# Optimization experiments

Measured on AMD Instinct MI355X. Metric: run time of the kernel, lower is better.

Reference implementation:

```python
import jax, jax.numpy as jnp
import numpy as np

DS = 8  # avg-pool / upsample factor

def _avg_pool(x, ds):
    B, C, H, W = x.shape
    return x.reshape(B, C, H // ds, ds, W // ds, ds).mean(axis=(3, 5))

def _conv1x1(x, W, b):
    # 1x1 conv == per-pixel channel matmul
    return jnp.einsum('bchw,oc->bohw', x, W) + b[None, :, None, None]

def setup_inputs() -> dict:
    key = jax.random.key(0)
    ks = jax.random.split(key, 8)
    B, C, H, W = 8, 64, 256, 256
    scale = 1.0 / np.sqrt(C)
    return {
        'x':    jax.random.normal(ks[0], (B, C, H, W), dtype=jnp.float32),
        'diff': jax.random.normal(ks[1], (B, C, H, W), dtype=jnp.float32),
        'Wq': jax.random.normal(ks[2], (C, C), dtype=jnp.float32) * scale,
        'bq': jax.random.normal(ks[3], (C,), dtype=jnp.float32) * 0.01,
        'Wk': jax.random.normal(ks[4], (C, C), dtype=jnp.float32) * scale,
        'bk': jax.random.normal(ks[5], (C,), dtype=jnp.float32) * 0.01,
        'Wv': jax.random.normal(ks[6], (C, C), dtype=jnp.float32) * scale,
        'bv': jax.random.normal(ks[7], (C,), dtype=jnp.float32) * 0.01,
    }

def reference(x, diff, Wq, bq, Wk, bk, Wv, bv):
    C = x.shape[1]
    d = _avg_pool(diff, DS)                 # [B,C,h,w]
    B, _, h, w = d.shape
    N = h * w
    q = _conv1x1(d, Wq, bq).reshape(B, C, N)
    k = _conv1x1(d, Wk, bk).reshape(B, C, N)
    # energy[b,n,m] = sum_c q[b,c,n] * k[b,c,m], scaled by C^-0.5
    energy = jnp.einsum('bcn,bcm->bnm', q, k) * (C ** -0.5)
    attn = jax.nn.softmax(energy, axis=-1)  # [B,N,N]
    v = _conv1x1(_avg_pool(x, DS), Wv, bv).reshape(B, C, N)
    # out = v @ attn^T  (torch: bmm(value, attention.permute(0,2,1)))
    out = jnp.einsum('bcm,bnm->bcn', v, attn).reshape(B, C, h, w)
    # F.interpolate nearest with exact integer factor == pixel repeat
    out = jnp.repeat(jnp.repeat(out, DS, axis=2), DS, axis=3)
    return out + x
```

## Files before the change

### kernel.cpp

```cpp
#include <hip/hip_runtime.h>

#define BB 8
#define CC 64
#define HH 256
#define WW 256
#define DSF 8
#define HP 32
#define WP 32
#define NN 1024

typedef _Float16 f16x4 __attribute__((ext_vector_type(4)));
typedef float f32x4 __attribute__((ext_vector_type(4)));

__global__ __launch_bounds__(256) void k_pool(const float* __restrict__ x,
                                              const float* __restrict__ diff,
                                              float* __restrict__ dpool,
                                              float* __restrict__ pxpool) {
    __shared__ float sums[256];
    int bid = blockIdx.x;
    int which = bid >> 14;
    int r = bid & 16383;
    int ph = r & 31;
    int c = (r >> 5) & 63;
    int b = r >> 11;
    const float* src = which ? x : diff;
    float* dst = which ? pxpool : dpool;
    const float* base = src + ((size_t)(b * CC + c) * HH + ph * DSF) * WW;
    int t = threadIdx.x;
    float s = 0.f;
#pragma unroll
    for (int kk = 0; kk < 2; ++kk) {
        int idx = t + kk * 256;
        int rr = idx >> 6;
        int j = idx & 63;
        float4 v = *(const float4*)(base + rr * WW + j * 4);
        s += v.x + v.y + v.z + v.w;
    }
    sums[t] = s;
    __syncthreads();
    if (t < 32) {
        float acc = 0.f;
#pragma unroll
        for (int rr = 0; rr < 4; ++rr)
            acc += sums[rr * 64 + 2 * t] + sums[rr * 64 + 2 * t + 1];
        dst[(size_t)(b * CC + c) * NN + ph * WP + t] = acc * (1.f / 64.f);
    }
}

__global__ __launch_bounds__(256) void k_proj(const float* __restrict__ dpool,
                                              const float* __restrict__ pxpool,
                                              const float* __restrict__ Wq, const float* __restrict__ bq,
                                              const float* __restrict__ Wk, const float* __restrict__ bk,
                                              const float* __restrict__ Wv, const float* __restrict__ bv,
                                              _Float16* __restrict__ qt, _Float16* __restrict__ kt,
                                              _Float16* __restrict__ vct) {
    __shared__ float Ws[64 * 65];
    __shared__ float dsh[64 * 68];
    int bid = blockIdx.x;
    int proj = bid >> 7;
    int rem = bid & 127;
    int b = rem >> 4;
    int n0 = (rem & 15) * 64;
    const float* Wm; const float* bias; const float* src;
    if (proj == 0)      { Wm = Wq; bias = bq; src = dpool; }
    else if (proj == 1) { Wm = Wk; bias = bk; src = dpool; }
    else                { Wm = Wv; bias = bv; src = pxpool; }
    int t = threadIdx.x;
#pragma unroll
    for (int i = 0; i < 16; ++i) {
        int e = t + i * 256;
        int o = e >> 6, c = e & 63;
        Ws[o * 65 + c] = Wm[e];
        dsh[o * 68 + c] = src[(size_t)(b * CC + o) * NN + n0 + c];
    }
    __syncthreads();
    int o = t & 63;
    int ng = t >> 6;
    float bb = bias[o];
    float4 acc[4];
#pragma unroll
    for (int j = 0; j < 4; ++j) acc[j] = make_float4(bb, bb, bb, bb);
#pragma unroll 8
    for (int c = 0; c < 64; ++c) {
        float wv = Ws[o * 65 + c];
        const float4* dr = (const float4*)(dsh + c * 68 + ng * 16);
#pragma unroll
        for (int j = 0; j < 4; ++j) {
            float4 d4 = dr[j];
            acc[j].x += wv * d4.x; acc[j].y += wv * d4.y;
            acc[j].z += wv * d4.z; acc[j].w += wv * d4.w;
        }
    }
    if (proj == 2) {
        _Float16* outp = vct + (size_t)(b * CC + o) * NN + n0 + ng * 16;
#pragma unroll
        for (int j = 0; j < 4; ++j) {
            f16x4 h;
            h[0] = (_Float16)acc[j].x; h[1] = (_Float16)acc[j].y;
            h[2] = (_Float16)acc[j].z; h[3] = (_Float16)acc[j].w;
            *(f16x4*)(outp + 4 * j) = h;
        }
    } else {
        __syncthreads();
#pragma unroll
        for (int j = 0; j < 4; ++j)
            *(float4*)(&dsh[o * 68 + ng * 16 + 4 * j]) = acc[j];
        __syncthreads();
        int nl = t & 63, og = t >> 6;
        float scale = (proj == 0) ? 0.125f : 1.0f;
        _Float16* outp = (proj == 0 ? qt : kt) + (size_t)(b * NN + n0 + nl) * CC + og * 16;
#pragma unroll
        for (int jj = 0; jj < 4; ++jj) {
            f16x4 h;
#pragma unroll
            for (int q4 = 0; q4 < 4; ++q4)
                h[q4] = (_Float16)(dsh[(og * 16 + 4 * jj + q4) * 68 + nl] * scale);
            *(f16x4*)(outp + 4 * jj) = h;
        }
    }
}

__global__ __launch_bounds__(256) void k_attn(const _Float16* __restrict__ qt,
                                              const _Float16* __restrict__ kt,
                                              const _Float16* __restrict__ vct,
                                              float* __restrict__ op) {
#define PS 1036
    __shared__ __align__(16) _Float16 P[16 * PS];
    __shared__ float part[4 * 16 * 65];
    __shared__ float wmax[4][16];
    __shared__ float wsum[4][16];
    int bid = blockIdx.x;
    int b = bid >> 6;
    int n0 = (bid & 63) * 16;
    int t = threadIdx.x;
    int w = t >> 6, l = t & 63;
    int lo = l & 15, g = l >> 4;

    const _Float16* qb = qt + (size_t)(b * NN + n0) * CC;
    const _Float16* kb = kt + (size_t)b * NN * CC;
    const _Float16* vb = vct + (size_t)b * CC * NN;

    f16x4 aq[4];
#pragma unroll
    for (int kc = 0; kc < 4; ++kc)
        aq[kc] = *(const f16x4*)(qb + lo * CC + 16 * kc + 4 * g);

    int mbase = w * 256;
    f32x4 e[16];
#pragma unroll
    for (int tm = 0; tm < 16; ++tm) e[tm] = (f32x4){0.f, 0.f, 0.f, 0.f};
#pragma unroll
    for (int tm = 0; tm < 16; ++tm) {
        int m = mbase + 16 * tm + lo;
        const _Float16* kr = kb + (size_t)m * CC + 4 * g;
#pragma unroll
        for (int kc = 0; kc < 4; ++kc) {
            f16x4 bk = *(const f16x4*)(kr + 16 * kc);
            e[tm] = __builtin_amdgcn_mfma_f32_16x16x16f16(aq[kc], bk, e[tm], 0, 0, 0);
        }
    }
    float mx[4], sm[4];
#pragma unroll
    for (int r = 0; r < 4; ++r) {
        float m_ = -1e30f;
#pragma unroll
        for (int tm = 0; tm < 16; ++tm) m_ = fmaxf(m_, e[tm][r]);
#pragma unroll
        for (int off = 8; off; off >>= 1) m_ = fmaxf(m_, __shfl_xor(m_, off));
        mx[r] = m_;
    }
    if (lo == 0) {
#pragma unroll
        for (int r = 0; r < 4; ++r) wmax[w][4 * g + r] = mx[r];
    }
    __syncthreads();
#pragma unroll
    for (int r = 0; r < 4; ++r) {
        int n = 4 * g + r;
        mx[r] = fmaxf(fmaxf(wmax[0][n], wmax[1][n]), fmaxf(wmax[2][n], wmax[3][n]));
        sm[r] = 0.f;
    }
#pragma unroll
    for (int tm = 0; tm < 16; ++tm) {
        int mcol = mbase + 16 * tm + lo;
#pragma unroll
        for (int r = 0; r < 4; ++r) {
            float p = __expf(e[tm][r] - mx[r]);
            sm[r] += p;
            P[(4 * g + r) * PS + mcol] = (_Float16)p;
        }
    }
#pragma unroll
    for (int r = 0; r < 4; ++r) {
#pragma unroll
        for (int off = 8; off; off >>= 1) sm[r] += __shfl_xor(sm[r], off);
    }
    if (lo == 0) {
#pragma unroll
        for (int r = 0; r < 4; ++r) wsum[w][4 * g + r] = sm[r];
    }
    f32x4 o4[4];
#pragma unroll
    for (int tc = 0; tc < 4; ++tc) o4[tc] = (f32x4){0.f, 0.f, 0.f, 0.f};
#pragma unroll
    for (int mk = 0; mk < 16; ++mk) {
        f16x4 pa = *(const f16x4*)(&P[lo * PS + mbase + 16 * mk + 4 * g]);
        const _Float16* vr = vb + mbase + 16 * mk + 4 * g;
#pragma unroll
        for (int tc = 0; tc < 4; ++tc) {
            f16x4 bv_ = *(const f16x4*)(vr + (size_t)(lo + 16 * tc) * NN);
            o4[tc] = __builtin_amdgcn_mfma_f32_16x16x16f16(pa, bv_, o4[tc], 0, 0, 0);
        }
    }
#pragma unroll
    for (int tc = 0; tc < 4; ++tc)
#pragma unroll
        for (int r = 0; r < 4; ++r)
            part[(w * 16 + 4 * g + r) * 65 + lo + 16 * tc] = o4[tc][r];
    __syncthreads();
#pragma unroll
    for (int i = 0; i < 4; ++i) {
        int e2 = t + i * 256;
        int c = e2 >> 4, n = e2 & 15;
        float s = part[(0 * 16 + n) * 65 + c] + part[(1 * 16 + n) * 65 + c] +
                  part[(2 * 16 + n) * 65 + c] + part[(3 * 16 + n) * 65 + c];
        float denom = wsum[0][n] + wsum[1][n] + wsum[2][n] + wsum[3][n];
        op[(size_t)(b * CC + c) * NN + n0 + n] = s / denom;
    }
#undef PS
}

__global__ __launch_bounds__(256) void k_out(const float* __restrict__ x,
                                             const float* __restrict__ op,
                                             float* __restrict__ out) {
    size_t gid = (size_t)blockIdx.x * 256 + threadIdx.x;
    size_t flat = gid * 4;
    int w = (int)(flat & 255);
    int h = (int)((flat >> 8) & 255);
    int bc = (int)(flat >> 16);
    float ov = op[(size_t)bc * NN + (h >> 3) * WP + (w >> 3)];
    float4 xv = *(const float4*)(x + flat);
    float4 r;
    r.x = xv.x + ov; r.y = xv.y + ov; r.z = xv.z + ov; r.w = xv.w + ov;
    *(float4*)(out + flat) = r;
}

extern "C" void kernel_launch(void* const* d_in, const int* in_sizes, int n_in,
                              void* d_out, int out_size, void* d_ws, size_t ws_size,
                              hipStream_t stream) {
    const float* x    = (const float*)d_in[0];
    const float* diff = (const float*)d_in[1];
    const float* Wq   = (const float*)d_in[2];
    const float* bq   = (const float*)d_in[3];
    const float* Wk   = (const float*)d_in[4];
    const float* bk   = (const float*)d_in[5];
    const float* Wv   = (const float*)d_in[6];
    const float* bv   = (const float*)d_in[7];
    float* ws = (float*)d_ws;
    float* dpool  = ws;
    float* pxpool = ws + 524288;
    float* op     = ws + 1048576;
    _Float16* qt  = (_Float16*)(ws + 1572864);
    _Float16* kt  = (_Float16*)(ws + 1835008);
    _Float16* vct = (_Float16*)(ws + 2097152);
    float* out = (float*)d_out;

    hipLaunchKernelGGL(k_pool, dim3(32768), dim3(256), 0, stream, x, diff, dpool, pxpool);
    hipLaunchKernelGGL(k_proj, dim3(384), dim3(256), 0, stream, dpool, pxpool,
                       Wq, bq, Wk, bk, Wv, bv, qt, kt, vct);
    hipLaunchKernelGGL(k_attn, dim3(512), dim3(256), 0, stream, qt, kt, vct, op);
    hipLaunchKernelGGL(k_out, dim3(32768), dim3(256), 0, stream, x, op, out);
}
```

Baseline: 135.1 us.

## Pool whole planes per block, use nontemporal loads for diff and stores for output

The pooling kernel now gives each block an entire 256x256 plane. Each wavefront does 8 row loads per pooled row and reduces with a shuffle instead of shared memory and a barrier, cutting the grid from 32768 to 1024 blocks. The diff input is read with nontemporal loads so it does not evict x, which is reused later; x is read normally to keep it cached for the output kernel. The output kernel handles two float4s per thread and writes with nontemporal stores. The risk is that fewer, larger blocks and cache-hint behaviour may lower memory parallelism or interact badly with the L2 and MALL.

```diff
diff --git a/kernel.cpp b/kernel.cpp
--- a/kernel.cpp
+++ b/kernel.cpp
@@ -16,34 +16,46 @@
                                               const float* __restrict__ diff,
                                               float* __restrict__ dpool,
                                               float* __restrict__ pxpool) {
-    __shared__ float sums[256];
     int bid = blockIdx.x;
-    int which = bid >> 14;
-    int r = bid & 16383;
-    int ph = r & 31;
-    int c = (r >> 5) & 63;
-    int b = r >> 11;
-    const float* src = which ? x : diff;
-    float* dst = which ? pxpool : dpool;
-    const float* base = src + ((size_t)(b * CC + c) * HH + ph * DSF) * WW;
-    int t = threadIdx.x;
-    float s = 0.f;
-#pragma unroll
-    for (int kk = 0; kk < 2; ++kk) {
-        int idx = t + kk * 256;
-        int rr = idx >> 6;
-        int j = idx & 63;
-        float4 v = *(const float4*)(base + rr * WW + j * 4);
-        s += v.x + v.y + v.z + v.w;
-    }
-    sums[t] = s;
-    __syncthreads();
-    if (t < 32) {
-        float acc = 0.f;
-#pragma unroll
-        for (int rr = 0; rr < 4; ++rr)
-            acc += sums[rr * 64 + 2 * t] + sums[rr * 64 + 2 * t + 1];
-        dst[(size_t)(b * CC + c) * NN + ph * WP + t] = acc * (1.f / 64.f);
+    int which = bid >> 9;
+    int plane = bid & 511;
+    const float* base = (which ? x : diff) + (size_t)plane * (HH * WW);
+    float* dst = (which ? pxpool : dpool) + (size_t)plane * NN;
+    int t = threadIdx.x;
+    int w = t >> 6, lane = t & 63;
+    if (which) {
+#pragma unroll 2
+        for (int pr = 0; pr < 8; ++pr) {
+            int row0 = (w * 8 + pr) * 8;
+            float4 r[8];
+#pragma unroll
+            for (int rr = 0; rr < 8; ++rr)
+                r[rr] = *(const float4*)(base + (size_t)(row0 + rr) * WW + lane * 4);
+            float s = 0.f;
+#pragma unroll
+            for (int rr = 0; rr < 8; ++rr)
+                s += (r[rr].x + r[rr].y) + (r[rr].z + r[rr].w);
+            s += __shfl_xor(s, 1);
+            if ((lane & 1) == 0)
+                dst[(w * 8 + pr) * 32 + (lane >> 1)] = s * (1.f / 64.f);
+        }
+    } else {
+#pragma unroll 2
+        for (int pr = 0; pr < 8; ++pr) {
+            int row0 = (w * 8 + pr) * 8;
+            f32x4 r[8];
+#pragma unroll
+            for (int rr = 0; rr < 8; ++rr)
+                r[rr] = __builtin_nontemporal_load(
+                    (const f32x4*)(base + (size_t)(row0 + rr) * WW + lane * 4));
+            float s = 0.f;
+#pragma unroll
+            for (int rr = 0; rr < 8; ++rr)
+                s += (r[rr][0] + r[rr][1]) + (r[rr][2] + r[rr][3]);
+            s += __shfl_xor(s, 1);
+            if ((lane & 1) == 0)
+                dst[(w * 8 + pr) * 32 + (lane >> 1)] = s * (1.f / 64.f);
+        }
     }
 }
 
@@ -233,16 +245,19 @@
 __global__ __launch_bounds__(256) void k_out(const float* __restrict__ x,
                                              const float* __restrict__ op,
                                              float* __restrict__ out) {
-    size_t gid = (size_t)blockIdx.x * 256 + threadIdx.x;
-    size_t flat = gid * 4;
-    int w = (int)(flat & 255);
-    int h = (int)((flat >> 8) & 255);
-    int bc = (int)(flat >> 16);
-    float ov = op[(size_t)bc * NN + (h >> 3) * WP + (w >> 3)];
-    float4 xv = *(const float4*)(x + flat);
-    float4 r;
-    r.x = xv.x + ov; r.y = xv.y + ov; r.z = xv.z + ov; r.w = xv.w + ov;
-    *(float4*)(out + flat) = r;
+    int t = threadIdx.x;
+#pragma unroll
+    for (int i = 0; i < 2; ++i) {
+        size_t idx4 = (size_t)blockIdx.x * 512 + i * 256 + t;
+        size_t flat = idx4 * 4;
+        int w = (int)(flat & 255);
+        int h = (int)((flat >> 8) & 255);
+        int bc = (int)(flat >> 16);
+        float ov = op[(size_t)bc * NN + (h >> 3) * WP + (w >> 3)];
+        float4 xv = *(const float4*)(x + flat);
+        f32x4 r = {xv.x + ov, xv.y + ov, xv.z + ov, xv.w + ov};
+        __builtin_nontemporal_store(r, (f32x4*)(out + flat));
+    }
 }
 
 extern "C" void kernel_launch(void* const* d_in, const int* in_sizes, int n_in,
@@ -265,9 +280,9 @@
     _Float16* vct = (_Float16*)(ws + 2097152);
     float* out = (float*)d_out;
 
-    hipLaunchKernelGGL(k_pool, dim3(32768), dim3(256), 0, stream, x, diff, dpool, pxpool);
+    hipLaunchKernelGGL(k_pool, dim3(1024), dim3(256), 0, stream, x, diff, dpool, pxpool);
     hipLaunchKernelGGL(k_proj, dim3(384), dim3(256), 0, stream, dpool, pxpool,
                        Wq, bq, Wk, bk, Wv, bv, qt, kt, vct);
     hipLaunchKernelGGL(k_attn, dim3(512), dim3(256), 0, stream, qt, kt, vct, op);
-    hipLaunchKernelGGL(k_out, dim3(32768), dim3(256), 0, stream, x, op, out);
-}
+    hipLaunchKernelGGL(k_out, dim3(16384), dim3(256), 0, stream, x, op, out);
+}
```

New measurement: 127.6 us. 5.5% less time.
